# Optimization experiments

Measured on AMD Instinct MI355X. Metric: run time of the kernel, lower is better.

Reference implementation:

```python
import jax, jax.numpy as jnp
import numpy as np
from jax import lax

V, E, H, SEQ = 50257, 512, 512, 2048
TAGS, START, STOP = 12, 10, 11
NEG = -10000.0


def _lstm_dir(x, Wih, Whh, bih, bhh, reverse):
    # x: [T, in], Wih: [4H, in], Whh: [4H, H] (torch gate order i,f,g,o)
    h0 = jnp.zeros((Whh.shape[1],), x.dtype)
    c0 = jnp.zeros((Whh.shape[1],), x.dtype)
    b = bih + bhh

    def step(carry, xt):
        h, c = carry
        gates = Wih @ xt + Whh @ h + b  # [4H]
        i, f, g, o = jnp.split(gates, 4)
        c = jax.nn.sigmoid(f) * c + jax.nn.sigmoid(i) * jnp.tanh(g)
        h = jax.nn.sigmoid(o) * jnp.tanh(c)
        return (h, c), h

    _, hs = lax.scan(step, (h0, c0), x, reverse=reverse)
    return hs  # [T, H]


def _bilstm_layer(x, Wih, Whh, bih, bhh):
    # stacked params: leading dim 2 = (fwd, bwd)
    fwd = _lstm_dir(x, Wih[0], Whh[0], bih[0], bhh[0], False)
    bwd = _lstm_dir(x, Wih[1], Whh[1], bih[1], bhh[1], True)
    return jnp.concatenate([fwd, bwd], axis=-1)  # [T, 2H]


def _viterbi(feats, transitions):
    # feats: [T, TAGS]; transitions[next, prev]
    init = jnp.full((TAGS,), NEG, feats.dtype).at[START].set(0.0)

    def step(fv, feat):
        scores = fv[None, :] + transitions  # [next, prev]
        bptr = jnp.argmax(scores, axis=1)
        fv_new = jnp.max(scores, axis=1) + feat
        return fv_new, bptr

    fv, bptrs = lax.scan(step, init, feats)
    terminal = fv + transitions[STOP]
    best_last = jnp.argmax(terminal)
    path_score = terminal[best_last]

    def back(tag, bp):
        prev = bp[tag]
        return prev, prev

    _, ys = lax.scan(back, best_last, bptrs, reverse=True)
    # ys[t] = path[t-1]; ys[0] = START (dropped); append best_last
    best_path = jnp.concatenate([ys[1:], best_last[None]])
    return path_score, best_path


def setup_inputs() -> dict:
    key = jax.random.key(0)
    ks = jax.random.split(key, 16)
    s = lambda *sh: 1.0 / np.sqrt(H)
    inp = {
        "sentence": jax.random.randint(ks[0], (SEQ,), 0, V),
        "emb": jax.random.normal(ks[1], (V, E), jnp.float32),
        "Wih0": jax.random.uniform(ks[2], (2, 4 * H, E), jnp.float32, -s(), s()),
        "Whh0": jax.random.uniform(ks[3], (2, 4 * H, H), jnp.float32, -s(), s()),
        "bih0": jax.random.uniform(ks[4], (2, 4 * H), jnp.float32, -s(), s()),
        "bhh0": jax.random.uniform(ks[5], (2, 4 * H), jnp.float32, -s(), s()),
        "Wih1": jax.random.uniform(ks[6], (2, 4 * H, 2 * H), jnp.float32, -s(), s()),
        "Whh1": jax.random.uniform(ks[7], (2, 4 * H, H), jnp.float32, -s(), s()),
        "bih1": jax.random.uniform(ks[8], (2, 4 * H), jnp.float32, -s(), s()),
        "bhh1": jax.random.uniform(ks[9], (2, 4 * H), jnp.float32, -s(), s()),
        "W_tag": jax.random.uniform(ks[10], (TAGS, 2 * H), jnp.float32, -0.1, 0.1),
        "b_tag": jnp.zeros((TAGS,), jnp.float32),
    }
    trans = jax.random.normal(ks[11], (TAGS, TAGS), jnp.float32)
    trans = trans.at[START, :].set(NEG).at[:, STOP].set(NEG)
    inp["transitions"] = trans
    return inp


def reference(sentence, emb, Wih0, Whh0, bih0, bhh0, Wih1, Whh1, bih1, bhh1, W_tag, b_tag, transitions):
    x = emb[sentence]  # [T, E]  (dropout identity in eval)
    x = _bilstm_layer(x, Wih0, Whh0, bih0, bhh0)
    x = _bilstm_layer(x, Wih1, Whh1, bih1, bhh1)
    feats = x @ W_tag.T + b_tag  # [T, TAGS]
    path_score, best_path = _viterbi(feats, transitions)
    return path_score, best_path
```

## Files before the change

### kernel.cpp

```cpp
#include <hip/hip_runtime.h>
#include <math.h>

#define SEQ 2048
#define EMB_D 512
#define HID 512
#define NTAGS 12
#define START_TAG 10
#define STOP_TAG 11
#define NEGV (-10000.0f)
#define POISON 0xAAAAAAAAu

__device__ __forceinline__ float sigf(float x) { return 1.0f / (1.0f + expf(-x)); }

__global__ void k_embed(const int* __restrict__ sent, const float* __restrict__ emb,
                        float* __restrict__ x0) {
    int t = blockIdx.x;
    int tid = threadIdx.x;
    int row = sent[t];
    const float4* src = (const float4*)(emb + (size_t)row * EMB_D);
    float4* dst = (float4*)(x0 + (size_t)t * EMB_D);
    dst[tid] = src[tid];
}

#define BM 64
#define BN 64
#define BKT 32
#define LDT 68

__global__ __launch_bounds__(256) void k_gemm(
    const float* __restrict__ Af, const float* __restrict__ Ab,
    const float* __restrict__ B,
    const float* __restrict__ biasA, const float* __restrict__ biasB,
    float* __restrict__ C, int K) {
    const int N = 2048;
    int dir = blockIdx.z;
    const float* Bd = B + (size_t)dir * N * K;
    const float* bA = biasA + dir * N;
    const float* bB = biasB + dir * N;
    float* Cd = C + (size_t)dir * 2048 * N;
    int m0 = blockIdx.y * BM, n0 = blockIdx.x * BN;

    __shared__ float As[BKT * LDT];
    __shared__ float Bs[BKT * LDT];

    int tid = threadIdx.x;
    int lrow = tid >> 2;
    int lk4 = (tid & 3) * 8;
    int tx = tid & 15, ty = tid >> 4;

    float acc[4][4] = {};

    for (int kt = 0; kt < K; kt += BKT) {
        {
            int m = m0 + lrow;
#pragma unroll
            for (int hh = 0; hh < 2; ++hh) {
                int k = kt + lk4 + hh * 4;
                const float* src = (k < 512) ? (Af + (size_t)m * 512 + k)
                                             : (Ab + (size_t)m * 512 + (k - 512));
                float4 v = *(const float4*)src;
                int kl = lk4 + hh * 4;
                As[(kl + 0) * LDT + lrow] = v.x;
                As[(kl + 1) * LDT + lrow] = v.y;
                As[(kl + 2) * LDT + lrow] = v.z;
                As[(kl + 3) * LDT + lrow] = v.w;
            }
        }
        {
            int n = n0 + lrow;
#pragma unroll
            for (int hh = 0; hh < 2; ++hh) {
                int k = kt + lk4 + hh * 4;
                float4 v = *(const float4*)(Bd + (size_t)n * K + k);
                int kl = lk4 + hh * 4;
                Bs[(kl + 0) * LDT + lrow] = v.x;
                Bs[(kl + 1) * LDT + lrow] = v.y;
                Bs[(kl + 2) * LDT + lrow] = v.z;
                Bs[(kl + 3) * LDT + lrow] = v.w;
            }
        }
        __syncthreads();
#pragma unroll
        for (int kk = 0; kk < BKT; ++kk) {
            float4 av = *(const float4*)&As[kk * LDT + ty * 4];
            float4 bv = *(const float4*)&Bs[kk * LDT + tx * 4];
            acc[0][0] += av.x * bv.x; acc[0][1] += av.x * bv.y; acc[0][2] += av.x * bv.z; acc[0][3] += av.x * bv.w;
            acc[1][0] += av.y * bv.x; acc[1][1] += av.y * bv.y; acc[1][2] += av.y * bv.z; acc[1][3] += av.y * bv.w;
            acc[2][0] += av.z * bv.x; acc[2][1] += av.z * bv.y; acc[2][2] += av.z * bv.z; acc[2][3] += av.z * bv.w;
            acc[3][0] += av.w * bv.x; acc[3][1] += av.w * bv.y; acc[3][2] += av.w * bv.z; acc[3][3] += av.w * bv.w;
        }
        __syncthreads();
    }
#pragma unroll
    for (int i = 0; i < 4; ++i) {
        int m = m0 + ty * 4 + i;
#pragma unroll
        for (int j = 0; j < 4; ++j) {
            int n = n0 + tx * 4 + j;
            Cd[(size_t)m * N + n] = acc[i][j] + bA[n] + bB[n];
        }
    }
}

__global__ __launch_bounds__(256, 1) void k_lstm(
    const float* __restrict__ Whh,
    const float* __restrict__ Gi,
    float* __restrict__ hstore)
{
    int wg = blockIdx.x;
    int dir = wg >> 5;
    int slice = wg & 31;
    int u_base = slice * 16;
    int tid = threadIdx.x;

    const float* Whh_d = Whh + (size_t)dir * 2048 * 512;
    const float* Gi_d = Gi + (size_t)dir * 2048 * 2048;
    float* h_d = hstore + (size_t)dir * 2048 * 512;

    int rl = tid >> 2;
    int kp = tid & 3;
    int gg = rl >> 4;
    int uu = rl & 15;
    int r = gg * 512 + u_base + uu;

    float w[128];
    {
        const float* wsrc = Whh_d + (size_t)r * 512 + kp * 128;
#pragma unroll
        for (int j = 0; j < 128; j += 4) {
            float4 v = *(const float4*)(wsrc + j);
            w[j] = v.x; w[j + 1] = v.y; w[j + 2] = v.z; w[j + 3] = v.w;
        }
    }

    __shared__ __align__(16) float hlds[512];
    __shared__ float gdot[64];
    float c_reg = 0.0f;

    for (int it = 0; it < 2048; ++it) {
        int t = dir ? (2047 - it) : it;

        float gi = 0.f;
        if (kp == 0) gi = Gi_d[(size_t)t * 2048 + r];

        if (it == 0) {
            ((float2*)hlds)[tid] = make_float2(0.f, 0.f);
        } else {
            int tprev = dir ? (t + 1) : (t - 1);
            const float* src = h_d + (size_t)tprev * 512 + 2 * tid;
            float a, b;
            do {
                a = __hip_atomic_load(src + 0, __ATOMIC_RELAXED, __HIP_MEMORY_SCOPE_AGENT);
                b = __hip_atomic_load(src + 1, __ATOMIC_RELAXED, __HIP_MEMORY_SCOPE_AGENT);
            } while (__float_as_uint(a) == POISON || __float_as_uint(b) == POISON);
            hlds[2 * tid] = a;
            hlds[2 * tid + 1] = b;
        }
        __syncthreads();

        float p = 0.f;
        const float4* h4 = (const float4*)hlds + kp * 32;
#pragma unroll
        for (int j4 = 0; j4 < 32; ++j4) {
            float4 hv = h4[j4];
            p += w[4 * j4 + 0] * hv.x;
            p += w[4 * j4 + 1] * hv.y;
            p += w[4 * j4 + 2] * hv.z;
            p += w[4 * j4 + 3] * hv.w;
        }
        p += __shfl_xor(p, 1);
        p += __shfl_xor(p, 2);
        if (kp == 0) gdot[rl] = p + gi;
        __syncthreads();

        if (tid < 16) {
            float iv = gdot[0 * 16 + tid];
            float fv = gdot[1 * 16 + tid];
            float gv = gdot[2 * 16 + tid];
            float ov = gdot[3 * 16 + tid];
            float c = sigf(fv) * c_reg + sigf(iv) * tanhf(gv);
            float h = sigf(ov) * tanhf(c);
            c_reg = c;
            __hip_atomic_store(h_d + (size_t)t * 512 + u_base + tid, h,
                               __ATOMIC_RELAXED, __HIP_MEMORY_SCOPE_AGENT);
        }
    }
}

__global__ __launch_bounds__(64) void k_feats(
    const float* __restrict__ h1,
    const float* __restrict__ Wt,
    const float* __restrict__ bt,
    float* __restrict__ feats)
{
    int t = blockIdx.x;
    int lane = threadIdx.x;
    __shared__ __align__(16) float xl[1024];
    const float4* hf = (const float4*)(h1 + (size_t)t * 512);
    const float4* hb = (const float4*)(h1 + (size_t)(2048 + t) * 512);
    ((float4*)xl)[lane] = hf[lane];
    ((float4*)xl)[lane + 64] = hf[lane + 64];
    ((float4*)xl)[128 + lane] = hb[lane];
    ((float4*)xl)[128 + lane + 64] = hb[lane + 64];
    __syncthreads();
    for (int tag = 0; tag < NTAGS; ++tag) {
        const float* wrow = Wt + tag * 1024;
        float s = 0.f;
        for (int k = lane; k < 1024; k += 64) s += xl[k] * wrow[k];
#pragma unroll
        for (int off = 32; off; off >>= 1) s += __shfl_xor(s, off);
        if (lane == 0) feats[t * NTAGS + tag] = s + bt[tag];
    }
}

__global__ __launch_bounds__(64) void k_viterbi(
    const float* __restrict__ feats, const float* __restrict__ trans,
    float* __restrict__ out) {
    __shared__ float fv[2][NTAGS];
    __shared__ unsigned char bp[SEQ * NTAGS];
    __shared__ float featbuf[256 * NTAGS];
    __shared__ float term[NTAGS];
    int lane = threadIdx.x;

    float tr[NTAGS];
    if (lane < NTAGS) {
#pragma unroll
        for (int p = 0; p < NTAGS; ++p) tr[p] = trans[lane * NTAGS + p];
        fv[0][lane] = (lane == START_TAG) ? 0.f : NEGV;
    }
    __syncthreads();

    int cur = 0;
    for (int tc = 0; tc < SEQ; tc += 256) {
        for (int i = lane; i < 256 * NTAGS; i += 64) featbuf[i] = feats[tc * NTAGS + i];
        __syncthreads();
        for (int tt = 0; tt < 256; ++tt) {
            int t = tc + tt;
            if (lane < NTAGS) {
                float best = fv[cur][0] + tr[0];
                int bi = 0;
#pragma unroll
                for (int p = 1; p < NTAGS; ++p) {
                    float s = fv[cur][p] + tr[p];
                    if (s > best) { best = s; bi = p; }
                }
                bp[t * NTAGS + lane] = (unsigned char)bi;
                fv[cur ^ 1][lane] = best + featbuf[tt * NTAGS + lane];
            }
            cur ^= 1;
            __syncthreads();
        }
    }

    if (lane < NTAGS) term[lane] = fv[cur][lane] + trans[STOP_TAG * NTAGS + lane];
    __syncthreads();
    if (lane == 0) {
        float best = term[0];
        int bi = 0;
        for (int p = 1; p < NTAGS; ++p) {
            if (term[p] > best) { best = term[p]; bi = p; }
        }
        out[0] = best;
        int tag = bi;
        out[1 + (SEQ - 1)] = (float)tag;
        for (int t = SEQ - 1; t >= 1; --t) {
            tag = bp[t * NTAGS + tag];
            out[t] = (float)tag;
        }
    }
}

extern "C" void kernel_launch(void* const* d_in, const int* in_sizes, int n_in,
                              void* d_out, int out_size, void* d_ws, size_t ws_size,
                              hipStream_t stream) {
    const int* sent = (const int*)d_in[0];
    const float* emb = (const float*)d_in[1];
    const float* Wih0 = (const float*)d_in[2];
    const float* Whh0 = (const float*)d_in[3];
    const float* bih0 = (const float*)d_in[4];
    const float* bhh0 = (const float*)d_in[5];
    const float* Wih1 = (const float*)d_in[6];
    const float* Whh1 = (const float*)d_in[7];
    const float* bih1 = (const float*)d_in[8];
    const float* bhh1 = (const float*)d_in[9];
    const float* Wtag = (const float*)d_in[10];
    const float* btag = (const float*)d_in[11];
    const float* trans = (const float*)d_in[12];
    float* out = (float*)d_out;

    char* ws = (char*)d_ws;
    size_t off = 0;
    auto alloc = [&](size_t bytes) {
        void* p = ws + off;
        off += (bytes + 255) & ~(size_t)255;
        return p;
    };
    float* x0 = (float*)alloc(2048ull * 512 * 4);
    float* Gi = (float*)alloc(2ull * 2048 * 2048 * 4);
    float* h0 = (float*)alloc(2ull * 2048 * 512 * 4);
    float* h1 = (float*)alloc(2ull * 2048 * 512 * 4);
    float* feats = (float*)alloc(2048ull * NTAGS * 4);

    hipMemsetAsync(h0, 0xAA, 2ull * 2048 * 512 * 4, stream);
    hipMemsetAsync(h1, 0xAA, 2ull * 2048 * 512 * 4, stream);

    k_embed<<<2048, 128, 0, stream>>>(sent, emb, x0);

    dim3 gg(32, 32, 2);
    k_gemm<<<gg, 256, 0, stream>>>(x0, x0, Wih0, bih0, bhh0, Gi, 512);
    k_lstm<<<64, 256, 0, stream>>>(Whh0, Gi, h0);
    k_gemm<<<gg, 256, 0, stream>>>(h0, h0 + 2048ull * 512, Wih1, bih1, bhh1, Gi, 1024);
    k_lstm<<<64, 256, 0, stream>>>(Whh1, Gi, h1);
    k_feats<<<2048, 64, 0, stream>>>(h1, Wtag, btag, feats);
    k_viterbi<<<1, 64, 0, stream>>>(feats, trans, out);
}
```

Before: 10.21 ms.

## Restructure LSTM recurrence to keep all gates per unit in one lane group

Each group of 16 lanes now holds all four gate rows of one hidden unit, so the gate dot products are finished with in-group shuffles and the cell update runs in registers. This removes the second block barrier and the shared-memory gate exchange on every timestep. The hidden-state buffer in shared memory is double buffered so the next step's writes cannot race with the current step's reads. Sigmoid and tanh switch to fast exp/divide approximations, which trades some accuracy for shorter latency on the serial critical path.

```diff
diff --git a/kernel.cpp b/kernel.cpp
--- a/kernel.cpp
+++ b/kernel.cpp
@@ -10,7 +10,12 @@
 #define NEGV (-10000.0f)
 #define POISON 0xAAAAAAAAu
 
-__device__ __forceinline__ float sigf(float x) { return 1.0f / (1.0f + expf(-x)); }
+__device__ __forceinline__ float sigf(float x) {
+    return __fdividef(1.f, 1.f + __expf(-x));
+}
+__device__ __forceinline__ float tanh_fast(float x) {
+    return 1.f - __fdividef(2.f, __expf(2.f * x) + 1.f);
+}
 
 __global__ void k_embed(const int* __restrict__ sent, const float* __restrict__ emb,
                         float* __restrict__ x0) {
@@ -112,76 +117,85 @@
     int slice = wg & 31;
     int u_base = slice * 16;
     int tid = threadIdx.x;
+    int uu = tid >> 4;
+    int q = tid & 15;
 
     const float* Whh_d = Whh + (size_t)dir * 2048 * 512;
     const float* Gi_d = Gi + (size_t)dir * 2048 * 2048;
     float* h_d = hstore + (size_t)dir * 2048 * 512;
 
-    int rl = tid >> 2;
-    int kp = tid & 3;
-    int gg = rl >> 4;
-    int uu = rl & 15;
-    int r = gg * 512 + u_base + uu;
-
     float w[128];
-    {
-        const float* wsrc = Whh_d + (size_t)r * 512 + kp * 128;
-#pragma unroll
-        for (int j = 0; j < 128; j += 4) {
+#pragma unroll
+    for (int g = 0; g < 4; ++g) {
+        const float* wsrc = Whh_d + (size_t)(g * 512 + u_base + uu) * 512 + q * 32;
+#pragma unroll
+        for (int j = 0; j < 32; j += 4) {
             float4 v = *(const float4*)(wsrc + j);
-            w[j] = v.x; w[j + 1] = v.y; w[j + 2] = v.z; w[j + 3] = v.w;
-        }
-    }
-
-    __shared__ __align__(16) float hlds[512];
-    __shared__ float gdot[64];
+            w[g * 32 + j + 0] = v.x;
+            w[g * 32 + j + 1] = v.y;
+            w[g * 32 + j + 2] = v.z;
+            w[g * 32 + j + 3] = v.w;
+        }
+    }
+#pragma unroll
+    for (int j = 0; j < 128; ++j) asm volatile("" : "+v"(w[j]));
+
+    __shared__ __align__(16) float hlds[2][512];
     float c_reg = 0.0f;
 
     for (int it = 0; it < 2048; ++it) {
         int t = dir ? (2047 - it) : it;
+        int b = it & 1;
 
         float gi = 0.f;
-        if (kp == 0) gi = Gi_d[(size_t)t * 2048 + r];
+        if (q < 4) gi = Gi_d[(size_t)t * 2048 + q * 512 + u_base + uu];
 
         if (it == 0) {
-            ((float2*)hlds)[tid] = make_float2(0.f, 0.f);
+            ((float2*)hlds[0])[tid] = make_float2(0.f, 0.f);
         } else {
             int tprev = dir ? (t + 1) : (t - 1);
             const float* src = h_d + (size_t)tprev * 512 + 2 * tid;
-            float a, b;
+            float a, bb;
             do {
                 a = __hip_atomic_load(src + 0, __ATOMIC_RELAXED, __HIP_MEMORY_SCOPE_AGENT);
-                b = __hip_atomic_load(src + 1, __ATOMIC_RELAXED, __HIP_MEMORY_SCOPE_AGENT);
-            } while (__float_as_uint(a) == POISON || __float_as_uint(b) == POISON);
-            hlds[2 * tid] = a;
-            hlds[2 * tid + 1] = b;
+                bb = __hip_atomic_load(src + 1, __ATOMIC_RELAXED, __HIP_MEMORY_SCOPE_AGENT);
+            } while (__float_as_uint(a) == POISON || __float_as_uint(bb) == POISON);
+            hlds[b][2 * tid] = a;
+            hlds[b][2 * tid + 1] = bb;
         }
         __syncthreads();
 
-        float p = 0.f;
-        const float4* h4 = (const float4*)hlds + kp * 32;
-#pragma unroll
-        for (int j4 = 0; j4 < 32; ++j4) {
+        float acc0 = 0.f, acc1 = 0.f, acc2 = 0.f, acc3 = 0.f;
+        const float4* h4 = (const float4*)(hlds[b] + q * 32);
+#pragma unroll
+        for (int j4 = 0; j4 < 8; ++j4) {
             float4 hv = h4[j4];
-            p += w[4 * j4 + 0] * hv.x;
-            p += w[4 * j4 + 1] * hv.y;
-            p += w[4 * j4 + 2] * hv.z;
-            p += w[4 * j4 + 3] * hv.w;
-        }
-        p += __shfl_xor(p, 1);
-        p += __shfl_xor(p, 2);
-        if (kp == 0) gdot[rl] = p + gi;
-        __syncthreads();
-
-        if (tid < 16) {
-            float iv = gdot[0 * 16 + tid];
-            float fv = gdot[1 * 16 + tid];
-            float gv = gdot[2 * 16 + tid];
-            float ov = gdot[3 * 16 + tid];
-            float c = sigf(fv) * c_reg + sigf(iv) * tanhf(gv);
-            float h = sigf(ov) * tanhf(c);
+            acc0 += w[0 * 32 + 4 * j4 + 0] * hv.x; acc0 += w[0 * 32 + 4 * j4 + 1] * hv.y;
+            acc0 += w[0 * 32 + 4 * j4 + 2] * hv.z; acc0 += w[0 * 32 + 4 * j4 + 3] * hv.w;
+            acc1 += w[1 * 32 + 4 * j4 + 0] * hv.x; acc1 += w[1 * 32 + 4 * j4 + 1] * hv.y;
+            acc1 += w[1 * 32 + 4 * j4 + 2] * hv.z; acc1 += w[1 * 32 + 4 * j4 + 3] * hv.w;
+            acc2 += w[2 * 32 + 4 * j4 + 0] * hv.x; acc2 += w[2 * 32 + 4 * j4 + 1] * hv.y;
+            acc2 += w[2 * 32 + 4 * j4 + 2] * hv.z; acc2 += w[2 * 32 + 4 * j4 + 3] * hv.w;
+            acc3 += w[3 * 32 + 4 * j4 + 0] * hv.x; acc3 += w[3 * 32 + 4 * j4 + 1] * hv.y;
+            acc3 += w[3 * 32 + 4 * j4 + 2] * hv.z; acc3 += w[3 * 32 + 4 * j4 + 3] * hv.w;
+        }
+        acc0 += (q == 0) ? gi : 0.f;
+        acc1 += (q == 1) ? gi : 0.f;
+        acc2 += (q == 2) ? gi : 0.f;
+        acc3 += (q == 3) ? gi : 0.f;
+#pragma unroll
+        for (int m = 1; m < 16; m <<= 1) {
+            acc0 += __shfl_xor(acc0, m);
+            acc1 += __shfl_xor(acc1, m);
+            acc2 += __shfl_xor(acc2, m);
+            acc3 += __shfl_xor(acc3, m);
+        }
+
+        if (q == 0) {
+            float c = sigf(acc1) * c_reg + sigf(acc0) * tanh_fast(acc2);
+            float h = sigf(acc3) * tanh_fast(c);
             c_reg = c;
-            __hip_atomic_store(h_d + (size_t)t * 512 + u_base + tid, h,
+            __hip_atomic_store(h_d + (size_t)t * 512 + u_base + uu, h,
                                __ATOMIC_RELAXED, __HIP_MEMORY_SCOPE_AGENT);
         }
     }
```

New measurement: 12.21 ms. 19.5% more time.
